# Kernel optimization log

Measured on AMD Instinct MI355X. Metric: run time of the kernel, lower is better.

Reference implementation:

```python
import jax, jax.numpy as jnp
import numpy as np

HIDDEN = 1024
N_HEADS = 16
HEAD_DIM = HIDDEN // N_HEADS


def apply_rope(x, freqs):
    # x: [b, s, h, d]; freqs: [s, d//2]
    b, s, h, d = x.shape
    x2 = x.reshape(b, s, h, d // 2, 2)
    x_real, x_imag = x2[..., 0], x2[..., 1]
    cos = jnp.cos(freqs)[None, :, None, :]  # [1, s, 1, d//2]
    sin = jnp.sin(freqs)[None, :, None, :]
    out_real = x_real * cos - x_imag * sin
    out_imag = x_real * sin + x_imag * cos
    return jnp.stack([out_real, out_imag], axis=-1).reshape(b, s, h, d)


def setup_inputs() -> dict:
    key = jax.random.key(0)
    k_x, k_f, k_wq, k_bq, k_wo, k_bo = jax.random.split(key, 6)
    b, s = 2, 2048
    x = jax.random.normal(k_x, (b, s, HIDDEN), dtype=jnp.float32)
    freqs = jax.random.normal(k_f, (s, HEAD_DIM // 2), dtype=jnp.float32)
    lim = 1.0 / np.sqrt(HIDDEN)
    W_qkv = jax.random.uniform(k_wq, (HIDDEN, 3 * HIDDEN), jnp.float32, -lim, lim)
    b_qkv = jax.random.uniform(k_bq, (3 * HIDDEN,), jnp.float32, -lim, lim)
    W_out = jax.random.uniform(k_wo, (HIDDEN, HIDDEN), jnp.float32, -lim, lim)
    b_out = jax.random.uniform(k_bo, (HIDDEN,), jnp.float32, -lim, lim)
    return {"x": x, "freqs": freqs, "W_qkv": W_qkv, "b_qkv": b_qkv,
            "W_out": W_out, "b_out": b_out}


def reference(x, freqs, W_qkv, b_qkv, W_out, b_out):
    b, s, c = x.shape
    h, d = N_HEADS, HEAD_DIM
    qkv = jnp.einsum('bsc,cf->bsf', x, W_qkv) + b_qkv  # [b, s, 3*c]
    qkv = qkv.reshape(b, s, 3, h, d)
    q, k, v = qkv[:, :, 0], qkv[:, :, 1], qkv[:, :, 2]  # [b, s, h, d]
    q = apply_rope(q, freqs)
    k = apply_rope(k, freqs)
    scale = 1.0 / np.sqrt(d).astype(np.float32)
    scores = jnp.einsum('bqhd,bkhd->bhqk', q, k) * scale  # [b, h, s, s]
    attn = jax.nn.softmax(scores, axis=-1)
    out = jnp.einsum('bhqk,bkhd->bqhd', attn, v).reshape(b, s, c)
    return jnp.einsum('bsc,cf->bsf', out, W_out) + b_out
```

## Files before the change

kernel.cpp:

```cpp
#include <hip/hip_runtime.h>
#include <math.h>

constexpr int kB = 2;
constexpr int kS = 2048;
constexpr int kC = 1024;
constexpr int kH = 16;
constexpr int kD = 64;
constexpr int kF = 3072;
constexpr int kT = kB * kS;

typedef __attribute__((ext_vector_type(8))) short short8v;
typedef __attribute__((ext_vector_type(4))) short short4v;
typedef __attribute__((ext_vector_type(4))) float f32x4;
typedef __attribute__((ext_vector_type(16))) float f32x16;

__device__ __forceinline__ short f2bf(float f) {
    unsigned u = __builtin_bit_cast(unsigned, f);
    u += 0x7fffu + ((u >> 16) & 1u);
    return (short)(u >> 16);
}

__device__ __forceinline__ unsigned cvtpk(float a, float b) {
    unsigned r;
    asm("v_cvt_pk_bf16_f32 %0, %1, %2" : "=v"(r) : "v"(a), "v"(b));
    return r;
}

__device__ __forceinline__ unsigned pk_bf16(float a, float b) {
    unsigned ua = __builtin_bit_cast(unsigned, a);
    ua += 0x7fffu + ((ua >> 16) & 1u);
    unsigned ub = __builtin_bit_cast(unsigned, b);
    ub += 0x7fffu + ((ub >> 16) & 1u);
    return (ua >> 16) | (ub & 0xffff0000u);
}

__device__ __forceinline__ void gl_lds16(const void* g, void* l) {
    __builtin_amdgcn_global_load_lds(
        (const __attribute__((address_space(1))) char*)g,
        (__attribute__((address_space(3))) char*)l, 16, 0, 0);
}

__device__ __forceinline__ f32x4 mfma16(short8v a, short8v b, f32x4 c) {
    return __builtin_amdgcn_mfma_f32_16x16x32_bf16(a, b, c, 0, 0, 0);
}
__device__ __forceinline__ f32x16 mfma32(short8v a, short8v b, f32x16 c) {
    return __builtin_amdgcn_mfma_f32_32x32x16_bf16(a, b, c, 0, 0, 0);
}

__device__ __forceinline__ void tcvt_body(const float* __restrict__ w,
                                          short* __restrict__ wt, int K, int N,
                                          int bx, int by, int t, float Ts[64][65]) {
    const int n0 = bx * 64, k0 = by * 64;
    const int r = t >> 4, c4 = (t & 15) * 4;
#pragma unroll
    for (int rr = 0; rr < 64; rr += 16) {
        float4 v = *reinterpret_cast<const float4*>(&w[(size_t)(k0 + r + rr) * N + n0 + c4]);
        Ts[r + rr][c4 + 0] = v.x; Ts[r + rr][c4 + 1] = v.y;
        Ts[r + rr][c4 + 2] = v.z; Ts[r + rr][c4 + 3] = v.w;
    }
    __syncthreads();
#pragma unroll
    for (int rr = 0; rr < 64; rr += 16) {
        int n = r + rr;
        short4v o = { f2bf(Ts[c4 + 0][n]), f2bf(Ts[c4 + 1][n]),
                      f2bf(Ts[c4 + 2][n]), f2bf(Ts[c4 + 3][n]) };
        *reinterpret_cast<short4v*>(&wt[(size_t)(n0 + n) * K + k0 + c4]) = o;
    }
}

__global__ __launch_bounds__(256) void prep_kernel(
    const float* __restrict__ x, short* __restrict__ xb,
    const float* __restrict__ wq, short* __restrict__ wqt,
    const float* __restrict__ wo, short* __restrict__ wot,
    const float* __restrict__ freqs, float* __restrict__ cost,
    float* __restrict__ sint) {
    __shared__ float Ts[64][65];
    const int bid = blockIdx.x, t = threadIdx.x;
    if (bid < 4096) {
        int i = bid * 256 + t;
        float4 v = reinterpret_cast<const float4*>(x)[i];
        short4v o = { f2bf(v.x), f2bf(v.y), f2bf(v.z), f2bf(v.w) };
        reinterpret_cast<short4v*>(xb)[i] = o;
    } else if (bid < 4864) {
        int i = bid - 4096;
        tcvt_body(wq, wqt, kC, kF, i % 48, i / 48, t, Ts);
    } else if (bid < 5120) {
        int i = bid - 4864;
        tcvt_body(wo, wot, kC, kC, i % 16, i / 16, t, Ts);
    } else {
        int i = (bid - 5120) * 256 + t;
        float f = freqs[i];
        float s, c;
        sincosf(f, &s, &c);
        cost[i] = c; sint[i] = s;
    }
}

__device__ __forceinline__ void gemm_main(const short* __restrict__ A,
                                          const short* __restrict__ Bt,
                                          int m0, int n0, short* Als, short* Bls,
                                          f32x4 acc[4][4]) {
    const int tid = threadIdx.x, wid = tid >> 6, lane = tid & 63;
    const int srow = lane >> 3, schunk = lane & 7;
    const int fr = lane & 15, fg = lane >> 4;
    const int wm = (wid >> 1) * 64, wn = (wid & 1) * 64;
    for (int kt = 0; kt < 1024; kt += 64) {
        __syncthreads();
#pragma unroll
        for (int j = 0; j < 4; ++j) {
            int i = wid * 4 + j;
            int row = i * 8 + srow;
            gl_lds16(&A[(size_t)(m0 + row) * 1024 + kt + ((schunk ^ (row & 7)) << 3)],
                     &Als[i * 512]);
        }
#pragma unroll
        for (int j = 0; j < 4; ++j) {
            int i = wid * 4 + j;
            int row = i * 8 + srow;
            gl_lds16(&Bt[(size_t)(n0 + row) * 1024 + kt + ((schunk ^ (row & 7)) << 3)],
                     &Bls[i * 512]);
        }
        __syncthreads();
#pragma unroll
        for (int kk = 0; kk < 2; ++kk) {
            short8v af[4], bf[4];
#pragma unroll
            for (int fm = 0; fm < 4; ++fm) {
                int row = wm + fm * 16 + fr;
                af[fm] = *reinterpret_cast<const short8v*>(
                    &Als[row * 64 + (((fg + 4 * kk) ^ (row & 7)) << 3)]);
            }
#pragma unroll
            for (int fn = 0; fn < 4; ++fn) {
                int row = wn + fn * 16 + fr;
                bf[fn] = *reinterpret_cast<const short8v*>(
                    &Bls[row * 64 + (((fg + 4 * kk) ^ (row & 7)) << 3)]);
            }
#pragma unroll
            for (int fm = 0; fm < 4; ++fm)
#pragma unroll
                for (int fn = 0; fn < 4; ++fn)
                    acc[fm][fn] = mfma16(af[fm], bf[fn], acc[fm][fn]);
        }
    }
}

__global__ __launch_bounds__(256) void qkv_gemm_kernel(
    const short* __restrict__ xb, const short* __restrict__ wqt,
    const float* __restrict__ bias, const float* __restrict__ cost,
    const float* __restrict__ sint,
    short* __restrict__ qg, short* __restrict__ kg, short* __restrict__ vt) {
    __shared__ __attribute__((aligned(16))) short Als[128 * 64];
    __shared__ __attribute__((aligned(16))) short Bls[128 * 64];
    f32x4 acc[4][4] = {};
    const int tid = threadIdx.x, wid = tid >> 6, lane = tid & 63;
    const int m0 = blockIdx.y * 128, n0 = blockIdx.x * 128;
    gemm_main(xb, wqt, m0, n0, Als, Bls, acc);

    const int fr = lane & 15, fg = lane >> 4;
    const int wm = (wid >> 1) * 64, wn = (wid & 1) * 64;
    const int which = (n0 + wn) >> 10;
    const int bidx = m0 >> 11;
#pragma unroll
    for (int fn = 0; fn < 4; ++fn) {
        int col = n0 + wn + fn * 16 + fr;
        float bv = bias[col];
        int d = col & 63;
        int h = (col >> 6) & 15;
        int p0 = d >> 1;
        int odd = d & 1;
#pragma unroll
        for (int fm = 0; fm < 4; ++fm) {
            int r0 = m0 + wm + fm * 16 + fg * 4;
            int s0 = r0 & 2047;
            float c[4];
#pragma unroll
            for (int r = 0; r < 4; ++r) c[r] = acc[fm][fn][r] + bv;
            if (which < 2) {
#pragma unroll
                for (int r = 0; r < 4; ++r) {
                    float cs = cost[(s0 + r) * 32 + p0];
                    float sn = sint[(s0 + r) * 32 + p0];
                    float p = __shfl_xor(c[r], 1);
                    float o = odd ? fmaf(p, sn, c[r] * cs) : fmaf(-p, sn, c[r] * cs);
                    c[r] = (which == 0) ? o * 0.1803368801f : o;
                }
                short* dst = which ? kg : qg;
                size_t base = ((size_t)(bidx * 16 + h) * 2048 + s0) * 64 + d;
#pragma unroll
                for (int r = 0; r < 4; ++r) dst[base + (size_t)r * 64] = f2bf(c[r]);
            } else {
                short4v o = { f2bf(c[0]), f2bf(c[1]), f2bf(c[2]), f2bf(c[3]) };
                *reinterpret_cast<short4v*>(
                    &vt[((size_t)(bidx * 16 + h) * 64 + d) * 2048 + s0]) = o;
            }
        }
    }
}

__global__ __launch_bounds__(256, 4) void attn_mfma_kernel(
    const short* __restrict__ qg, const short* __restrict__ kg,
    const short* __restrict__ vt, short* __restrict__ ab) {
    __shared__ __attribute__((aligned(16))) short LDSBUF[16384];
    const int tid = threadIdx.x, wid = tid >> 6, lane = tid & 63;
    const int l31 = lane & 31, hi = lane >> 5;
    const int p = wid >> 1;
    const int wq = wid & 1;
    const int r8 = lane >> 3, c8 = lane & 7;
    const int soff = 8 * (c8 ^ r8);

    const int bid = blockIdx.x;
    const int swz = (bid & 7) * 128 + (bid >> 3);
    const int bh = swz >> 5;
    const int q0 = (swz & 31) * 64 + wq * 32;

    const short* qb = qg + (size_t)bh * 2048 * 64;
    const short* kb = kg + (size_t)bh * 2048 * 64;
    const short* vb = vt + (size_t)bh * 64 * 2048;

    short8v qf[4];
#pragma unroll
    for (int kkq = 0; kkq < 4; ++kkq)
        qf[kkq] = *reinterpret_cast<const short8v*>(
            &qb[(size_t)(q0 + l31) * 64 + kkq * 16 + hi * 8]);

    f32x16 o[2] = {};
    float l_i = 0.f;

    auto stage = [&](int t, int buf) {
        const int kt = t * 32;
        short* Kd = LDSBUF + buf * 8192 + p * 2048 + (wq * 8) * 64;
        const short* Ks = kb + (size_t)(p * 1024 + kt) * 64;
#pragma unroll
        for (int j = 0; j < 2; ++j) {
            int row = j * 16 + wq * 8 + r8;
            gl_lds16(Ks + (size_t)row * 64 + soff, Kd + j * 1024);
        }
        short* Vd = LDSBUF + buf * 8192 + 4096 + (wid * 8) * 64;
        const int s = c8 ^ r8;
#pragma unroll
        for (int j = 0; j < 2; ++j) {
            int d = j * 32 + wid * 8 + r8;
            gl_lds16(vb + (size_t)d * 2048 + (s >> 2) * 1024 + kt + (s & 3) * 8,
                     Vd + j * 2048);
        }
    };

    stage(0, 0);
    __syncthreads();

    for (int t = 0; t < 32; ++t) {
        const int buf = t & 1;
        if (t + 1 < 32) stage(t + 1, buf ^ 1);
        const short* Kb = LDSBUF + buf * 8192 + p * 2048;
        const short* Vb = LDSBUF + buf * 8192 + 4096;

        f32x16 sacc = {};
#pragma unroll
        for (int kkq = 0; kkq < 4; ++kkq) {
            short8v a = *reinterpret_cast<const short8v*>(
                &Kb[l31 * 64 + (((kkq * 2 + hi) ^ (l31 & 7)) << 3)]);
            sacc = mfma32(a, qf[kkq], sacc);
        }

#pragma unroll
        for (int r = 0; r < 16; ++r) sacc[r] = __builtin_amdgcn_exp2f(sacc[r]);
        float t8[8];
#pragma unroll
        for (int r = 0; r < 8; ++r) t8[r] = sacc[r] + sacc[r + 8];
        float t4[4];
#pragma unroll
        for (int r = 0; r < 4; ++r) t4[r] = t8[r] + t8[r + 4];
        float rs = (t4[0] + t4[1]) + (t4[2] + t4[3]);
        rs += __shfl_xor(rs, 32);
        l_i += rs;

        unsigned c[8];
#pragma unroll
        for (int i = 0; i < 8; ++i) c[i] = cvtpk(sacc[2 * i], sacc[2 * i + 1]);
        short8v pb[2];
#pragma unroll
        for (int kk = 0; kk < 2; ++kk) {
            unsigned a0 = c[kk * 4 + 0], a1 = c[kk * 4 + 1];
            unsigned a2 = c[kk * 4 + 2], a3 = c[kk * 4 + 3];
            unsigned s0x = (unsigned)__shfl_xor((int)a0, 32);
            unsigned s1x = (unsigned)__shfl_xor((int)a1, 32);
            unsigned s2x = (unsigned)__shfl_xor((int)a2, 32);
            unsigned s3x = (unsigned)__shfl_xor((int)a3, 32);
            uint4 w;
            w.x = hi ? s2x : a0;
            w.y = hi ? s3x : a1;
            w.z = hi ? a2 : s0x;
            w.w = hi ? a3 : s1x;
            pb[kk] = __builtin_bit_cast(short8v, w);
        }

#pragma unroll
        for (int kk = 0; kk < 2; ++kk) {
            short8v v0 = *reinterpret_cast<const short8v*>(
                &Vb[l31 * 64 + (((p * 4 + kk * 2 + hi) ^ (l31 & 7)) << 3)]);
            short8v v1 = *reinterpret_cast<const short8v*>(
                &Vb[(32 + l31) * 64 + (((p * 4 + kk * 2 + hi) ^ (l31 & 7)) << 3)]);
            o[0] = mfma32(v0, pb[kk], o[0]);
            o[1] = mfma32(v1, pb[kk], o[1]);
        }
        __syncthreads();
    }

    float* olds = reinterpret_cast<float*>(LDSBUF + 4096);
    float* lls  = olds + 2 * 2304;
    if (p == 1) {
        float* ob = olds + wq * 2304 + lane * 36;
#pragma unroll
        for (int i = 0; i < 4; ++i) {
            f32x4 w0 = { o[0][4 * i + 0], o[0][4 * i + 1], o[0][4 * i + 2], o[0][4 * i + 3] };
            *reinterpret_cast<f32x4*>(ob + i * 4) = w0;
            f32x4 w1 = { o[1][4 * i + 0], o[1][4 * i + 1], o[1][4 * i + 2], o[1][4 * i + 3] };
            *reinterpret_cast<f32x4*>(ob + 16 + i * 4) = w1;
        }
        lls[wq * 64 + lane] = l_i;
    }
    __syncthreads();
    if (p == 0) {
        float* ob = olds + wq * 2304 + lane * 36;
#pragma unroll
        for (int i = 0; i < 4; ++i) {
            f32x4 w0 = *reinterpret_cast<const f32x4*>(ob + i * 4);
            f32x4 w1 = *reinterpret_cast<const f32x4*>(ob + 16 + i * 4);
#pragma unroll
            for (int j = 0; j < 4; ++j) {
                o[0][4 * i + j] += w0[j];
                o[1][4 * i + j] += w1[j];
            }
        }
        l_i += lls[wq * 64 + lane];

        const float inv = 1.f / l_i;
        short* ep = LDSBUF + wid * 2048;
        const int q = l31;
#pragma unroll
        for (int fd = 0; fd < 2; ++fd)
#pragma unroll
            for (int i = 0; i < 4; ++i) {
                int d0 = fd * 32 + 8 * i + 4 * hi;
                uint2 w;
                w.x = pk_bf16(o[fd][4 * i + 0] * inv, o[fd][4 * i + 1] * inv);
                w.y = pk_bf16(o[fd][4 * i + 2] * inv, o[fd][4 * i + 3] * inv);
                *reinterpret_cast<uint2*>(&ep[q * 64 + (d0 ^ (8 * (q & 3)))]) = w;
            }
        __builtin_amdgcn_s_waitcnt(0);
        const int bb = bh >> 4, hh = bh & 15;
        const int wrow = r8, wcol = c8;
#pragma unroll
        for (int j = 0; j < 4; ++j) {
            int row = j * 8 + wrow;
            short8v tv = *reinterpret_cast<const short8v*>(
                &ep[row * 64 + ((8 * wcol) ^ (8 * (row & 3)))]);
            int s = q0 + row;
            *reinterpret_cast<short8v*>(
                &ab[(size_t)(bb * 2048 + s) * 1024 + hh * 64 + 8 * wcol]) = tv;
        }
    }
}

__global__ __launch_bounds__(256) void out_gemm_kernel(
    const short* __restrict__ ab, const short* __restrict__ wot,
    const float* __restrict__ bias, float* __restrict__ out) {
    __shared__ __attribute__((aligned(16))) short Als[128 * 64];
    __shared__ __attribute__((aligned(16))) short Bls[64 * 64];
    f32x4 acc[4][2] = {};
    const int tid = threadIdx.x, wid = tid >> 6, lane = tid & 63;
    const int srow = lane >> 3, schunk = lane & 7;
    const int fr = lane & 15, fg = lane >> 4;
    const int wm = (wid >> 1) * 64, wn = (wid & 1) * 32;
    const int m0 = blockIdx.y * 128, n0 = blockIdx.x * 64;

    for (int kt = 0; kt < 1024; kt += 64) {
        __syncthreads();
#pragma unroll
        for (int j = 0; j < 4; ++j) {
            int i = wid * 4 + j;
            int row = i * 8 + srow;
            gl_lds16(&ab[(size_t)(m0 + row) * 1024 + kt + ((schunk ^ (row & 7)) << 3)],
                     &Als[i * 512]);
        }
#pragma unroll
        for (int j = 0; j < 2; ++j) {
            int i = wid * 2 + j;
            int row = i * 8 + srow;
            gl_lds16(&wot[(size_t)(n0 + row) * 1024 + kt + ((schunk ^ (row & 7)) << 3)],
                     &Bls[i * 512]);
        }
        __syncthreads();
#pragma unroll
        for (int kk = 0; kk < 2; ++kk) {
            short8v af[4], bf[2];
#pragma unroll
            for (int fm = 0; fm < 4; ++fm) {
                int row = wm + fm * 16 + fr;
                af[fm] = *reinterpret_cast<const short8v*>(
                    &Als[row * 64 + (((fg + 4 * kk) ^ (row & 7)) << 3)]);
            }
#pragma unroll
            for (int fn = 0; fn < 2; ++fn) {
                int row = wn + fn * 16 + fr;
                bf[fn] = *reinterpret_cast<const short8v*>(
                    &Bls[row * 64 + (((fg + 4 * kk) ^ (row & 7)) << 3)]);
            }
#pragma unroll
            for (int fm = 0; fm < 4; ++fm)
#pragma unroll
                for (int fn = 0; fn < 2; ++fn)
                    acc[fm][fn] = mfma16(af[fm], bf[fn], acc[fm][fn]);
        }
    }
#pragma unroll
    for (int fn = 0; fn < 2; ++fn) {
        int col = n0 + wn + fn * 16 + fr;
        float bv = bias[col];
#pragma unroll
        for (int fm = 0; fm < 4; ++fm) {
            int r0 = m0 + wm + fm * 16 + fg * 4;
#pragma unroll
            for (int r = 0; r < 4; ++r)
                out[(size_t)(r0 + r) * 1024 + col] = acc[fm][fn][r] + bv;
        }
    }
}

extern "C" void kernel_launch(void* const* d_in, const int* in_sizes, int n_in,
                              void* d_out, int out_size, void* d_ws, size_t ws_size,
                              hipStream_t stream) {
    const float* x     = (const float*)d_in[0];
    const float* freqs = (const float*)d_in[1];
    const float* W_qkv = (const float*)d_in[2];
    const float* b_qkv = (const float*)d_in[3];
    const float* W_out = (const float*)d_in[4];
    const float* b_out = (const float*)d_in[5];
    float* out = (float*)d_out;

    char* w = (char*)d_ws;
    short* xb  = (short*)w;  w += (size_t)kT * kC * 2;
    short* wqt = (short*)w;  w += (size_t)kF * kC * 2;
    short* wot = (short*)w;  w += (size_t)kC * kC * 2;
    short* qgw = (short*)w;  w += (size_t)kB * kH * kS * kD * 2;
    short* kgw = (short*)w;  w += (size_t)kB * kH * kS * kD * 2;
    short* vtw = (short*)w;  w += (size_t)kB * kH * kS * kD * 2;
    short* abw = (short*)w;  w += (size_t)kT * kC * 2;
    float* costt = (float*)w; w += (size_t)kS * (kD / 2) * 4;
    float* sintt = (float*)w; w += (size_t)kS * (kD / 2) * 4;

    prep_kernel<<<dim3(5376), 256, 0, stream>>>(x, xb, W_qkv, wqt, W_out, wot,
                                                freqs, costt, sintt);
    qkv_gemm_kernel<<<dim3(kF / 128, kT / 128), 256, 0, stream>>>(
        xb, wqt, b_qkv, costt, sintt, qgw, kgw, vtw);
    attn_mfma_kernel<<<dim3(1024), 256, 0, stream>>>(qgw, kgw, vtw, abw);
    out_gemm_kernel<<<dim3(kC / 64, kT / 128), 256, 0, stream>>>(abw, wot, b_out, out);
}
```

Before: 126.1 us.

## Fuse x fp32-to-bf16 conversion into QKV GEMM and use permlane32 swap in attention

The separate prep pass that converted x to bf16 is removed. The QKV GEMM now streams fp32 x tiles straight into LDS with a swizzled layout and converts them to bf16 when loading fragments. This drops a full write and read of the bf16 activation buffer, but doubles LDS traffic and footprint for the A tile and repeats the conversion in every column block (24x). Separately, the attention kernel's half-wave exchange of P fragments now uses v_permlane32_swap instead of four shuffles and selects.

After: 136.7 us. 8.4% more time.

```diff
diff --git a/kernel.cpp b/kernel.cpp
--- a/kernel.cpp
+++ b/kernel.cpp
@@ -26,6 +26,10 @@
     return r;
 }
 
+__device__ __forceinline__ void plane32_swap(unsigned& a, unsigned& b) {
+    asm volatile("v_permlane32_swap_b32 %0, %1" : "+v"(a), "+v"(b));
+}
+
 __device__ __forceinline__ unsigned pk_bf16(float a, float b) {
     unsigned ua = __builtin_bit_cast(unsigned, a);
     ua += 0x7fffu + ((ua >> 16) & 1u);
@@ -69,30 +73,124 @@
 }
 
 __global__ __launch_bounds__(256) void prep_kernel(
-    const float* __restrict__ x, short* __restrict__ xb,
     const float* __restrict__ wq, short* __restrict__ wqt,
     const float* __restrict__ wo, short* __restrict__ wot,
     const float* __restrict__ freqs, float* __restrict__ cost,
     float* __restrict__ sint) {
     __shared__ float Ts[64][65];
     const int bid = blockIdx.x, t = threadIdx.x;
-    if (bid < 4096) {
-        int i = bid * 256 + t;
-        float4 v = reinterpret_cast<const float4*>(x)[i];
-        short4v o = { f2bf(v.x), f2bf(v.y), f2bf(v.z), f2bf(v.w) };
-        reinterpret_cast<short4v*>(xb)[i] = o;
-    } else if (bid < 4864) {
-        int i = bid - 4096;
-        tcvt_body(wq, wqt, kC, kF, i % 48, i / 48, t, Ts);
-    } else if (bid < 5120) {
-        int i = bid - 4864;
+    if (bid < 768) {
+        tcvt_body(wq, wqt, kC, kF, bid % 48, bid / 48, t, Ts);
+    } else if (bid < 1024) {
+        int i = bid - 768;
         tcvt_body(wo, wot, kC, kC, i % 16, i / 16, t, Ts);
     } else {
-        int i = (bid - 5120) * 256 + t;
+        int i = (bid - 1024) * 256 + t;
         float f = freqs[i];
         float s, c;
         sincosf(f, &s, &c);
         cost[i] = c; sint[i] = s;
+    }
+}
+
+__global__ __launch_bounds__(256) void qkv_gemm_kernel(
+    const float* __restrict__ x, const short* __restrict__ wqt,
+    const float* __restrict__ bias, const float* __restrict__ cost,
+    const float* __restrict__ sint,
+    short* __restrict__ qg, short* __restrict__ kg, short* __restrict__ vt) {
+    __shared__ __attribute__((aligned(16))) float Afls[128 * 64];
+    __shared__ __attribute__((aligned(16))) short Bls[128 * 64];
+    f32x4 acc[4][4] = {};
+    const int tid = threadIdx.x, wid = tid >> 6, lane = tid & 63;
+    const int fr = lane & 15, fg = lane >> 4;
+    const int wm = (wid >> 1) * 64, wn = (wid & 1) * 64;
+    const int m0 = blockIdx.y * 128, n0 = blockIdx.x * 128;
+    const int br = lane >> 3, bc = lane & 7;
+
+    for (int kt = 0; kt < 1024; kt += 64) {
+        __syncthreads();
+#pragma unroll
+        for (int j = 0; j < 8; ++j) {
+            int flat = (wid * 8 + j) * 64 + lane;
+            int row = flat >> 4, pos = flat & 15;
+            gl_lds16(&x[(size_t)(m0 + row) * 1024 + kt + ((pos ^ ((row & 7) << 1)) << 2)],
+                     &Afls[(wid * 8 + j) * 256]);
+        }
+#pragma unroll
+        for (int j = 0; j < 4; ++j) {
+            int i = wid * 4 + j;
+            int brow = i * 8 + br;
+            gl_lds16(&wqt[(size_t)(n0 + brow) * 1024 + kt + ((bc ^ (brow & 7)) << 3)],
+                     &Bls[i * 512]);
+        }
+        __syncthreads();
+#pragma unroll
+        for (int kk = 0; kk < 2; ++kk) {
+            short8v af[4], bf[4];
+#pragma unroll
+            for (int fm = 0; fm < 4; ++fm) {
+                int row = wm + fm * 16 + fr;
+                int cs = ((fg + 4 * kk) * 2) ^ ((row & 7) << 1);
+                const float* pA = &Afls[row * 64 + cs * 4];
+                f32x4 lo = *reinterpret_cast<const f32x4*>(pA);
+                f32x4 hi4 = *reinterpret_cast<const f32x4*>(pA + 4);
+                uint4 u;
+                u.x = cvtpk(lo[0], lo[1]);
+                u.y = cvtpk(lo[2], lo[3]);
+                u.z = cvtpk(hi4[0], hi4[1]);
+                u.w = cvtpk(hi4[2], hi4[3]);
+                af[fm] = __builtin_bit_cast(short8v, u);
+            }
+#pragma unroll
+            for (int fn = 0; fn < 4; ++fn) {
+                int row = wn + fn * 16 + fr;
+                bf[fn] = *reinterpret_cast<const short8v*>(
+                    &Bls[row * 64 + (((fg + 4 * kk) ^ (row & 7)) << 3)]);
+            }
+#pragma unroll
+            for (int fm = 0; fm < 4; ++fm)
+#pragma unroll
+                for (int fn = 0; fn < 4; ++fn)
+                    acc[fm][fn] = mfma16(af[fm], bf[fn], acc[fm][fn]);
+        }
+    }
+
+    const int which = (n0 + wn) >> 10;
+    const int bidx = m0 >> 11;
+#pragma unroll
+    for (int fn = 0; fn < 4; ++fn) {
+        int col = n0 + wn + fn * 16 + fr;
+        float bv = bias[col];
+        int d = col & 63;
+        int h = (col >> 6) & 15;
+        int p0 = d >> 1;
+        int odd = d & 1;
+#pragma unroll
+        for (int fm = 0; fm < 4; ++fm) {
+            int r0 = m0 + wm + fm * 16 + fg * 4;
+            int s0 = r0 & 2047;
+            float c[4];
+#pragma unroll
+            for (int r = 0; r < 4; ++r) c[r] = acc[fm][fn][r] + bv;
+            if (which < 2) {
+#pragma unroll
+                for (int r = 0; r < 4; ++r) {
+                    float cs = cost[(s0 + r) * 32 + p0];
+                    float sn = sint[(s0 + r) * 32 + p0];
+                    float p = __shfl_xor(c[r], 1);
+                    float o = odd ? fmaf(p, sn, c[r] * cs) : fmaf(-p, sn, c[r] * cs);
+                    c[r] = (which == 0) ? o * 0.1803368801f : o;
+                }
+                short* dst = which ? kg : qg;
+                size_t base = ((size_t)(bidx * 16 + h) * 2048 + s0) * 64 + d;
+#pragma unroll
+                for (int r = 0; r < 4; ++r) dst[base + (size_t)r * 64] = f2bf(c[r]);
+            } else {
+                short4v o = { f2bf(c[0]), f2bf(c[1]), f2bf(c[2]), f2bf(c[3]) };
+                *reinterpret_cast<short4v*>(
+                    &vt[((size_t)(bidx * 16 + h) * 64 + d) * 2048 + s0]) = o;
+            }
+        }
     }
 }
 
@@ -141,59 +239,6 @@
 #pragma unroll
                 for (int fn = 0; fn < 4; ++fn)
                     acc[fm][fn] = mfma16(af[fm], bf[fn], acc[fm][fn]);
-        }
-    }
-}
-
-__global__ __launch_bounds__(256) void qkv_gemm_kernel(
-    const short* __restrict__ xb, const short* __restrict__ wqt,
-    const float* __restrict__ bias, const float* __restrict__ cost,
-    const float* __restrict__ sint,
-    short* __restrict__ qg, short* __restrict__ kg, short* __restrict__ vt) {
-    __shared__ __attribute__((aligned(16))) short Als[128 * 64];
-    __shared__ __attribute__((aligned(16))) short Bls[128 * 64];
-    f32x4 acc[4][4] = {};
-    const int tid = threadIdx.x, wid = tid >> 6, lane = tid & 63;
-    const int m0 = blockIdx.y * 128, n0 = blockIdx.x * 128;
-    gemm_main(xb, wqt, m0, n0, Als, Bls, acc);
-
-    const int fr = lane & 15, fg = lane >> 4;
-    const int wm = (wid >> 1) * 64, wn = (wid & 1) * 64;
-    const int which = (n0 + wn) >> 10;
-    const int bidx = m0 >> 11;
-#pragma unroll
-    for (int fn = 0; fn < 4; ++fn) {
-        int col = n0 + wn + fn * 16 + fr;
-        float bv = bias[col];
-        int d = col & 63;
-        int h = (col >> 6) & 15;
-        int p0 = d >> 1;
-        int odd = d & 1;
-#pragma unroll
-        for (int fm = 0; fm < 4; ++fm) {
-            int r0 = m0 + wm + fm * 16 + fg * 4;
-            int s0 = r0 & 2047;
-            float c[4];
-#pragma unroll
-            for (int r = 0; r < 4; ++r) c[r] = acc[fm][fn][r] + bv;
-            if (which < 2) {
-#pragma unroll
-                for (int r = 0; r < 4; ++r) {
-                    float cs = cost[(s0 + r) * 32 + p0];
-                    float sn = sint[(s0 + r) * 32 + p0];
-                    float p = __shfl_xor(c[r], 1);
-                    float o = odd ? fmaf(p, sn, c[r] * cs) : fmaf(-p, sn, c[r] * cs);
-                    c[r] = (which == 0) ? o * 0.1803368801f : o;
-                }
-                short* dst = which ? kg : qg;
-                size_t base = ((size_t)(bidx * 16 + h) * 2048 + s0) * 64 + d;
-#pragma unroll
-                for (int r = 0; r < 4; ++r) dst[base + (size_t)r * 64] = f2bf(c[r]);
-            } else {
-                short4v o = { f2bf(c[0]), f2bf(c[1]), f2bf(c[2]), f2bf(c[3]) };
-                *reinterpret_cast<short4v*>(
-                    &vt[((size_t)(bidx * 16 + h) * 64 + d) * 2048 + s0]) = o;
-            }
         }
     }
 }
@@ -281,17 +326,12 @@
         short8v pb[2];
 #pragma unroll
         for (int kk = 0; kk < 2; ++kk) {
-            unsigned a0 = c[kk * 4 + 0], a1 = c[kk * 4 + 1];
-            unsigned a2 = c[kk * 4 + 2], a3 = c[kk * 4 + 3];
-            unsigned s0x = (unsigned)__shfl_xor((int)a0, 32);
-            unsigned s1x = (unsigned)__shfl_xor((int)a1, 32);
-            unsigned s2x = (unsigned)__shfl_xor((int)a2, 32);
-            unsigned s3x = (unsigned)__shfl_xor((int)a3, 32);
+            unsigned x0 = c[4 * kk + 0], y0 = c[4 * kk + 2];
+            unsigned x1 = c[4 * kk + 1], y1 = c[4 * kk + 3];
+            plane32_swap(x0, y0);
+            plane32_swap(x1, y1);
             uint4 w;
-            w.x = hi ? s2x : a0;
-            w.y = hi ? s3x : a1;
-            w.z = hi ? a2 : s0x;
-            w.w = hi ? a3 : s1x;
+            w.x = x0; w.y = x1; w.z = y0; w.w = y1;
             pb[kk] = __builtin_bit_cast(short8v, w);
         }
 
@@ -440,7 +480,6 @@
     float* out = (float*)d_out;
 
     char* w = (char*)d_ws;
-    short* xb  = (short*)w;  w += (size_t)kT * kC * 2;
     short* wqt = (short*)w;  w += (size_t)kF * kC * 2;
     short* wot = (short*)w;  w += (size_t)kC * kC * 2;
     short* qgw = (short*)w;  w += (size_t)kB * kH * kS * kD * 2;
@@ -450,10 +489,10 @@
     float* costt = (float*)w; w += (size_t)kS * (kD / 2) * 4;
     float* sintt = (float*)w; w += (size_t)kS * (kD / 2) * 4;
 
-    prep_kernel<<<dim3(5376), 256, 0, stream>>>(x, xb, W_qkv, wqt, W_out, wot,
+    prep_kernel<<<dim3(1280), 256, 0, stream>>>(W_qkv, wqt, W_out, wot,
                                                 freqs, costt, sintt);
     qkv_gemm_kernel<<<dim3(kF / 128, kT / 128), 256, 0, stream>>>(
-        xb, wqt, b_qkv, costt, sintt, qgw, kgw, vtw);
+        x, wqt, b_qkv, costt, sintt, qgw, kgw, vtw);
     attn_mfma_kernel<<<dim3(1024), 256, 0, stream>>>(qgw, kgw, vtw, abw);
     out_gemm_kernel<<<dim3(kC / 64, kT / 128), 256, 0, stream>>>(abw, wot, b_out, out);
 }
```
